# Kernel optimization log

Measured on AMD Instinct MI355X. Metric: run time of the kernel, lower is better.

The kernel has to match this reference:

```python
import jax, jax.numpy as jnp
import numpy as np

B, TQ, TKV = 2, 2048, 2048
Q_IN, KV_IN, D_MODEL, N_HEADS = 1024, 1024, 1024, 16
D_HEAD = D_MODEL // N_HEADS


def setup_inputs() -> dict:
    key = jax.random.key(0)
    ks = jax.random.split(key, 12)
    s_q = 1.0 / np.sqrt(Q_IN)
    s_kv = 1.0 / np.sqrt(KV_IN)
    s_o = 1.0 / np.sqrt(D_MODEL)
    return {
        "q": jax.random.normal(ks[0], (B, TQ, Q_IN), jnp.float32),
        "kv": jax.random.normal(ks[1], (B, TKV, KV_IN), jnp.float32),
        "mask": jnp.triu(jnp.ones((TQ, TKV), jnp.bool_), k=1),  # True = masked
        "Wq": jax.random.uniform(ks[2], (D_MODEL, Q_IN), jnp.float32, -s_q, s_q),
        "bq": jax.random.uniform(ks[3], (D_MODEL,), jnp.float32, -s_q, s_q),
        "Wk": jax.random.uniform(ks[4], (D_HEAD, KV_IN), jnp.float32, -s_kv, s_kv),
        "bk": jax.random.uniform(ks[5], (D_HEAD,), jnp.float32, -s_kv, s_kv),
        "Wv": jax.random.uniform(ks[6], (D_HEAD, KV_IN), jnp.float32, -s_kv, s_kv),
        "bv": jax.random.uniform(ks[7], (D_HEAD,), jnp.float32, -s_kv, s_kv),
        "Wo": jax.random.uniform(ks[8], (D_MODEL, D_MODEL), jnp.float32, -s_o, s_o),
        "bo": jax.random.uniform(ks[9], (D_MODEL,), jnp.float32, -s_o, s_o),
    }


def reference(q, kv, mask, Wq, bq, Wk, bk, Wv, bv, Wo, bo):
    b, tq, _ = q.shape
    scale = jnp.sqrt(jnp.asarray(D_HEAD, q.dtype))
    # Q: [B, H, Tq, Dh]; K/V: single shared head [B, Tkv, Dh]
    Q = (q @ Wq.T + bq).reshape(b, tq, N_HEADS, D_HEAD).transpose(0, 2, 1, 3)
    K = kv @ Wk.T + bk
    V = kv @ Wv.T + bv
    scores = jnp.einsum("bhqd,bkd->bhqk", Q, K) / scale
    scores = jnp.where(mask[None, None, :, :], -jnp.inf, scores)
    attn_weights = jax.nn.softmax(scores, axis=-1)  # dropout is identity (eval / p=0)
    attended = jnp.einsum("bhqk,bkd->bhqd", attn_weights, V)
    attended = attended.transpose(0, 2, 1, 3).reshape(b, tq, D_MODEL)
    out = attended @ Wo.T + bo
    return out, attn_weights
```

## Files before the change

### kernel.cpp

```cpp
#include <hip/hip_runtime.h>

#define BATCH 2
#define TQ 2048
#define TKV 2048
#define DMODEL 1024
#define NHEADS 16
#define DHEAD 64
#define KIN 1024

typedef __attribute__((ext_vector_type(4))) float f32x4;
typedef __attribute__((ext_vector_type(8))) short bf16x8;

#define MFMA16(a, b, c) __builtin_amdgcn_mfma_f32_16x16x32_bf16(a, b, c, 0, 0, 0)

__device__ inline short f2bf(float f) {
    unsigned u = __builtin_bit_cast(unsigned, f);
    unsigned r = u + 0x7FFFu + ((u >> 16) & 1u);
    return (short)(r >> 16);
}
__device__ inline bf16x8 cvt8v(f32x4 lo, f32x4 hi) {
    bf16x8 r;
    r[0] = f2bf(lo[0]); r[1] = f2bf(lo[1]); r[2] = f2bf(lo[2]); r[3] = f2bf(lo[3]);
    r[4] = f2bf(hi[0]); r[5] = f2bf(hi[1]); r[6] = f2bf(hi[2]); r[7] = f2bf(hi[3]);
    return r;
}

template<bool A_F32, bool OUT_F32>
__global__ __launch_bounds__(256) void gemm_bt_bias(
    const void* __restrict__ Av, const float* __restrict__ B,
    const float* __restrict__ bias, void* __restrict__ Cv,
    int M, int N, int K)
{
    __shared__ short As[128 * 40];
    __shared__ short Bs[128 * 40];
    const int tid = threadIdx.x;
    const int lane = tid & 63, wave = tid >> 6;
    const int quad = lane >> 4, l16 = lane & 15;
    const int wm = wave & 1, wn = wave >> 1;
    const int mBase = blockIdx.x * 128, nBase = blockIdx.y * 128;

    f32x4 acc[4][4];
#pragma unroll
    for (int i = 0; i < 4; i++)
#pragma unroll
        for (int j = 0; j < 4; j++) acc[i][j] = (f32x4){0.f, 0.f, 0.f, 0.f};

    const int r0 = tid >> 2;
    const int c0 = (tid & 3) * 8;

    for (int k0 = 0; k0 < K; k0 += 32) {
        bf16x8 a0, a1, b0, b1;
        if constexpr (A_F32) {
            const float* Af = (const float*)Av;
            const f32x4* p0 = (const f32x4*)&Af[(size_t)(mBase + r0) * K + k0 + c0];
            const f32x4* p1 = (const f32x4*)&Af[(size_t)(mBase + r0 + 64) * K + k0 + c0];
            a0 = cvt8v(p0[0], p0[1]);
            a1 = cvt8v(p1[0], p1[1]);
        } else {
            const short* Ab = (const short*)Av;
            a0 = *(const bf16x8*)&Ab[(size_t)(mBase + r0) * K + k0 + c0];
            a1 = *(const bf16x8*)&Ab[(size_t)(mBase + r0 + 64) * K + k0 + c0];
        }
        {
            const f32x4* q0 = (const f32x4*)&B[(size_t)(nBase + r0) * K + k0 + c0];
            const f32x4* q1 = (const f32x4*)&B[(size_t)(nBase + r0 + 64) * K + k0 + c0];
            b0 = cvt8v(q0[0], q0[1]);
            b1 = cvt8v(q1[0], q1[1]);
        }
        __syncthreads();
        *(bf16x8*)&As[r0 * 40 + c0] = a0;
        *(bf16x8*)&As[(r0 + 64) * 40 + c0] = a1;
        *(bf16x8*)&Bs[r0 * 40 + c0] = b0;
        *(bf16x8*)&Bs[(r0 + 64) * 40 + c0] = b1;
        __syncthreads();
        bf16x8 af[4], bfr[4];
#pragma unroll
        for (int mt = 0; mt < 4; mt++)
            af[mt] = *(const bf16x8*)&As[(wm * 64 + mt * 16 + l16) * 40 + quad * 8];
#pragma unroll
        for (int nt = 0; nt < 4; nt++)
            bfr[nt] = *(const bf16x8*)&Bs[(wn * 64 + nt * 16 + l16) * 40 + quad * 8];
#pragma unroll
        for (int mt = 0; mt < 4; mt++)
#pragma unroll
            for (int nt = 0; nt < 4; nt++)
                acc[mt][nt] = MFMA16(af[mt], bfr[nt], acc[mt][nt]);
    }

#pragma unroll
    for (int nt = 0; nt < 4; nt++) {
        int col = nBase + wn * 64 + nt * 16 + l16;
        float bv = bias[col];
#pragma unroll
        for (int mt = 0; mt < 4; mt++) {
            int row = mBase + wm * 64 + mt * 16 + quad * 4;
#pragma unroll
            for (int r = 0; r < 4; r++) {
                float val = acc[mt][nt][r] + bv;
                size_t idx = (size_t)(row + r) * N + col;
                if constexpr (OUT_F32) ((float*)Cv)[idx] = val;
                else                   ((short*)Cv)[idx] = f2bf(val);
            }
        }
    }
}

__global__ __launch_bounds__(256) void kvproj(
    const float* __restrict__ A,
    const float* __restrict__ Wk, const float* __restrict__ bkp,
    const float* __restrict__ Wv, const float* __restrict__ bvp,
    short* __restrict__ Kout,
    short* __restrict__ Vt)
{
    const int K = KIN;
    __shared__ short As[128 * 40];
    __shared__ short Bs[128 * 40];
    const int tid = threadIdx.x;
    const int lane = tid & 63, wave = tid >> 6;
    const int quad = lane >> 4, l16 = lane & 15;
    const int wm = wave & 1, wn = wave >> 1;
    const int mBase = blockIdx.x * 128;

    f32x4 acc[4][4];
#pragma unroll
    for (int i = 0; i < 4; i++)
#pragma unroll
        for (int j = 0; j < 4; j++) acc[i][j] = (f32x4){0.f, 0.f, 0.f, 0.f};

    const int r0 = tid >> 2;
    const int c0 = (tid & 3) * 8;

    for (int k0 = 0; k0 < K; k0 += 32) {
        const f32x4* p0 = (const f32x4*)&A[(size_t)(mBase + r0) * K + k0 + c0];
        const f32x4* p1 = (const f32x4*)&A[(size_t)(mBase + r0 + 64) * K + k0 + c0];
        const f32x4* q0 = (const f32x4*)&Wk[(size_t)r0 * K + k0 + c0];
        const f32x4* q1 = (const f32x4*)&Wv[(size_t)r0 * K + k0 + c0];
        bf16x8 a0 = cvt8v(p0[0], p0[1]);
        bf16x8 a1 = cvt8v(p1[0], p1[1]);
        bf16x8 b0 = cvt8v(q0[0], q0[1]);
        bf16x8 b1 = cvt8v(q1[0], q1[1]);
        __syncthreads();
        *(bf16x8*)&As[r0 * 40 + c0] = a0;
        *(bf16x8*)&As[(r0 + 64) * 40 + c0] = a1;
        *(bf16x8*)&Bs[r0 * 40 + c0] = b0;
        *(bf16x8*)&Bs[(r0 + 64) * 40 + c0] = b1;
        __syncthreads();
        bf16x8 af[4], bfr[4];
#pragma unroll
        for (int mt = 0; mt < 4; mt++)
            af[mt] = *(const bf16x8*)&As[(wm * 64 + mt * 16 + l16) * 40 + quad * 8];
#pragma unroll
        for (int nt = 0; nt < 4; nt++)
            bfr[nt] = *(const bf16x8*)&Bs[(wn * 64 + nt * 16 + l16) * 40 + quad * 8];
#pragma unroll
        for (int mt = 0; mt < 4; mt++)
#pragma unroll
            for (int nt = 0; nt < 4; nt++)
                acc[mt][nt] = MFMA16(af[mt], bfr[nt], acc[mt][nt]);
    }

#pragma unroll
    for (int nt = 0; nt < 4; nt++) {
        int n = wn * 64 + nt * 16 + l16;
        float bv = (n < 64) ? bkp[n] : bvp[n - 64];
#pragma unroll
        for (int mt = 0; mt < 4; mt++) {
            int row = mBase + wm * 64 + mt * 16 + quad * 4;
#pragma unroll
            for (int r = 0; r < 4; r++) {
                short v = f2bf(acc[mt][nt][r] + bv);
                int m = row + r;
                if (n < 64) {
                    Kout[(size_t)m * 64 + n] = v;
                } else {
                    int b = m >> 11, t = m & 2047;
                    Vt[((size_t)(b * 64 + (n - 64))) * 2048 + t] = v;
                }
            }
        }
    }
}

__global__ __launch_bounds__(256) void attn_core(
    const short* __restrict__ Qbuf,
    const short* __restrict__ Kbuf,
    const short* __restrict__ Vt,
    float* __restrict__ attnW,
    short* __restrict__ attOut)
{
    const int blk = blockIdx.x;
    const int qb = blk & 31;
    const int h = (blk >> 5) & 15;
    const int b = blk >> 9;
    const int lane = threadIdx.x & 63, wave = threadIdx.x >> 6;
    const int quad = lane >> 4, l16 = lane & 15;
    const int qrow0 = qb * 64 + wave * 16;

    __shared__ short EsAll[4][16 * 72];
    __shared__ float PsAll[4][16 * 68];
    short* Es = &EsAll[wave][0];
    float* Ps = &PsAll[wave][0];

    const short* qp = Qbuf + (size_t)(b * TQ + qrow0 + l16) * DMODEL + h * 64;
    bf16x8 aq[2];
    aq[0] = *(const bf16x8*)(qp + quad * 8);
    aq[1] = *(const bf16x8*)(qp + 32 + quad * 8);

    const short* Kb = Kbuf + (size_t)b * TKV * DHEAD;
    const short* Vb = Vt + (size_t)b * DHEAD * TKV;

    f32x4 attacc[4];
#pragma unroll
    for (int i = 0; i < 4; i++) attacc[i] = (f32x4){0.f, 0.f, 0.f, 0.f};
    float rowsum[4] = {0.f, 0.f, 0.f, 0.f};

    for (int kb = 0; kb <= qb; ++kb) {
        f32x4 s[4];
#pragma unroll
        for (int i = 0; i < 4; i++) s[i] = (f32x4){0.f, 0.f, 0.f, 0.f};
#pragma unroll
        for (int nt = 0; nt < 4; nt++) {
            const short* kp = Kb + (size_t)(kb * 64 + nt * 16 + l16) * DHEAD + quad * 8;
            bf16x8 k0 = *(const bf16x8*)kp;
            bf16x8 k1 = *(const bf16x8*)(kp + 32);
            s[nt] = MFMA16(aq[0], k0, s[nt]);
            s[nt] = MFMA16(aq[1], k1, s[nt]);
        }
        const bool diag = (kb == qb);
#pragma unroll
        for (int nt = 0; nt < 4; nt++) {
            int col = kb * 64 + nt * 16 + l16;
#pragma unroll
            for (int r = 0; r < 4; r++) {
                int row = qrow0 + quad * 4 + r;
                float e = (diag && col > row) ? 0.f : __expf(s[nt][r] * 0.125f);
                rowsum[r] += e;
                Es[(quad * 4 + r) * 72 + nt * 16 + l16] = f2bf(e);
            }
        }
        __syncthreads();
        bf16x8 ae0 = *(const bf16x8*)&Es[l16 * 72 + quad * 8];
        bf16x8 ae1 = *(const bf16x8*)&Es[l16 * 72 + 32 + quad * 8];
#pragma unroll
        for (int dt = 0; dt < 4; dt++) {
            const short* vp = Vb + (size_t)(dt * 16 + l16) * TKV + kb * 64 + quad * 8;
            bf16x8 v0 = *(const bf16x8*)vp;
            bf16x8 v1 = *(const bf16x8*)(vp + 32);
            attacc[dt] = MFMA16(ae0, v0, attacc[dt]);
            attacc[dt] = MFMA16(ae1, v1, attacc[dt]);
        }
        __syncthreads();
    }

#pragma unroll
    for (int r = 0; r < 4; r++) {
#pragma unroll
        for (int m = 1; m < 16; m <<= 1) rowsum[r] += __shfl_xor(rowsum[r], m, 64);
    }
    float rinv[4];
#pragma unroll
    for (int r = 0; r < 4; r++) rinv[r] = 1.f / rowsum[r];

#pragma unroll
    for (int dt = 0; dt < 4; dt++) {
#pragma unroll
        for (int r = 0; r < 4; r++) {
            size_t idx = (size_t)(b * TQ + qrow0 + quad * 4 + r) * DMODEL + h * 64 + dt * 16 + l16;
            attOut[idx] = f2bf(attacc[dt][r] * rinv[r]);
        }
    }

    float* Wrow = attnW + (size_t)(b * NHEADS + h) * TQ * TKV;
    const int srow = lane >> 2;
    const int sc = (lane & 3) * 16;
    const f32x4 zz = {0.f, 0.f, 0.f, 0.f};

    for (int kb = 0; kb < TKV / 64; ++kb) {
        float* gp = Wrow + (size_t)(qrow0 + srow) * TKV + kb * 64 + sc;
        if (kb > qb) {
            ((f32x4*)gp)[0] = zz; ((f32x4*)gp)[1] = zz;
            ((f32x4*)gp)[2] = zz; ((f32x4*)gp)[3] = zz;
        } else {
            f32x4 s[4];
#pragma unroll
            for (int i = 0; i < 4; i++) s[i] = (f32x4){0.f, 0.f, 0.f, 0.f};
#pragma unroll
            for (int nt = 0; nt < 4; nt++) {
                const short* kp = Kb + (size_t)(kb * 64 + nt * 16 + l16) * DHEAD + quad * 8;
                bf16x8 k0 = *(const bf16x8*)kp;
                bf16x8 k1 = *(const bf16x8*)(kp + 32);
                s[nt] = MFMA16(aq[0], k0, s[nt]);
                s[nt] = MFMA16(aq[1], k1, s[nt]);
            }
            const bool diag = (kb == qb);
#pragma unroll
            for (int nt = 0; nt < 4; nt++) {
                int col = kb * 64 + nt * 16 + l16;
#pragma unroll
                for (int r = 0; r < 4; r++) {
                    int row = qrow0 + quad * 4 + r;
                    float e = (diag && col > row) ? 0.f
                              : __expf(s[nt][r] * 0.125f) * rinv[r];
                    Ps[(quad * 4 + r) * 68 + nt * 16 + l16] = e;
                }
            }
            __syncthreads();
            f32x4 w0 = ((const f32x4*)&Ps[srow * 68 + sc])[0];
            f32x4 w1 = ((const f32x4*)&Ps[srow * 68 + sc])[1];
            f32x4 w2 = ((const f32x4*)&Ps[srow * 68 + sc])[2];
            f32x4 w3 = ((const f32x4*)&Ps[srow * 68 + sc])[3];
            ((f32x4*)gp)[0] = w0; ((f32x4*)gp)[1] = w1;
            ((f32x4*)gp)[2] = w2; ((f32x4*)gp)[3] = w3;
            __syncthreads();
        }
    }
}

extern "C" void kernel_launch(void* const* d_in, const int* in_sizes, int n_in,
                              void* d_out, int out_size, void* d_ws, size_t ws_size,
                              hipStream_t stream) {
    const float* q  = (const float*)d_in[0];
    const float* kv = (const float*)d_in[1];
    const float* Wq = (const float*)d_in[3];
    const float* bq = (const float*)d_in[4];
    const float* Wk = (const float*)d_in[5];
    const float* bk = (const float*)d_in[6];
    const float* Wv = (const float*)d_in[7];
    const float* bv = (const float*)d_in[8];
    const float* Wo = (const float*)d_in[9];
    const float* bo = (const float*)d_in[10];

    float* out   = (float*)d_out;
    float* attnW = out + (size_t)BATCH * TQ * DMODEL;

    short* Qbuf = (short*)d_ws;
    short* Kbuf = Qbuf + (size_t)BATCH * TQ * DMODEL;
    short* Vtb  = Kbuf + (size_t)BATCH * TKV * DHEAD;
    short* Att  = Vtb + (size_t)BATCH * DHEAD * TKV;

    dim3 blk(256);
    gemm_bt_bias<true, false><<<dim3(32, 8), blk, 0, stream>>>(
        q, Wq, bq, Qbuf, BATCH * TQ, DMODEL, KIN);
    kvproj<<<dim3(32, 1), blk, 0, stream>>>(kv, Wk, bk, Wv, bv, Kbuf, Vtb);
    attn_core<<<dim3(BATCH * NHEADS * (TQ / 64)), blk, 0, stream>>>(
        Qbuf, Kbuf, Vtb, attnW, Att);
    gemm_bt_bias<false, true><<<dim3(32, 8), blk, 0, stream>>>(
        Att, Wo, bo, out, BATCH * TQ, DMODEL, DMODEL);
}
```

Baseline: 1.056 ms.

## Shrink GEMM tiles, reverse attention block order, drop barriers, nontemporal weight stores

The projection GEMMs shrink to 128x64 tiles and kvproj to 64-row tiles, doubling grid sizes so more blocks fill the CUs. Attention blocks are launched heaviest-first by reversing the query-block index. The per-wave shared buffers are aliased and the block-wide barriers between per-wave stages are removed. Attention-weight writes become nontemporal row-strided stores. Removing barriers relies on each wave touching only its own shared region, and the smaller tiles re-read operands more often.

```diff
diff --git a/kernel.cpp b/kernel.cpp
--- a/kernel.cpp
+++ b/kernel.cpp
@@ -26,30 +26,32 @@
 }
 
 template<bool A_F32, bool OUT_F32>
-__global__ __launch_bounds__(256) void gemm_bt_bias(
+__global__ __launch_bounds__(256, 2) void gemm_bt_bias(
     const void* __restrict__ Av, const float* __restrict__ B,
     const float* __restrict__ bias, void* __restrict__ Cv,
     int M, int N, int K)
 {
     __shared__ short As[128 * 40];
-    __shared__ short Bs[128 * 40];
+    __shared__ short Bs[64 * 40];
     const int tid = threadIdx.x;
     const int lane = tid & 63, wave = tid >> 6;
     const int quad = lane >> 4, l16 = lane & 15;
     const int wm = wave & 1, wn = wave >> 1;
-    const int mBase = blockIdx.x * 128, nBase = blockIdx.y * 128;
-
-    f32x4 acc[4][4];
+    const int mBase = blockIdx.x * 128, nBase = blockIdx.y * 64;
+
+    f32x4 acc[4][2];
 #pragma unroll
     for (int i = 0; i < 4; i++)
 #pragma unroll
-        for (int j = 0; j < 4; j++) acc[i][j] = (f32x4){0.f, 0.f, 0.f, 0.f};
+        for (int j = 0; j < 2; j++) acc[i][j] = (f32x4){0.f, 0.f, 0.f, 0.f};
 
     const int r0 = tid >> 2;
     const int c0 = (tid & 3) * 8;
+    const int rB = tid & 63;
+    const int cB = (tid >> 6) * 8;
 
     for (int k0 = 0; k0 < K; k0 += 32) {
-        bf16x8 a0, a1, b0, b1;
+        bf16x8 a0, a1, b0;
         if constexpr (A_F32) {
             const float* Af = (const float*)Av;
             const f32x4* p0 = (const f32x4*)&Af[(size_t)(mBase + r0) * K + k0 + c0];
@@ -62,34 +64,31 @@
             a1 = *(const bf16x8*)&Ab[(size_t)(mBase + r0 + 64) * K + k0 + c0];
         }
         {
-            const f32x4* q0 = (const f32x4*)&B[(size_t)(nBase + r0) * K + k0 + c0];
-            const f32x4* q1 = (const f32x4*)&B[(size_t)(nBase + r0 + 64) * K + k0 + c0];
+            const f32x4* q0 = (const f32x4*)&B[(size_t)(nBase + rB) * K + k0 + cB];
             b0 = cvt8v(q0[0], q0[1]);
-            b1 = cvt8v(q1[0], q1[1]);
         }
         __syncthreads();
         *(bf16x8*)&As[r0 * 40 + c0] = a0;
         *(bf16x8*)&As[(r0 + 64) * 40 + c0] = a1;
-        *(bf16x8*)&Bs[r0 * 40 + c0] = b0;
-        *(bf16x8*)&Bs[(r0 + 64) * 40 + c0] = b1;
+        *(bf16x8*)&Bs[rB * 40 + cB] = b0;
         __syncthreads();
-        bf16x8 af[4], bfr[4];
+        bf16x8 af[4], bfr[2];
 #pragma unroll
         for (int mt = 0; mt < 4; mt++)
             af[mt] = *(const bf16x8*)&As[(wm * 64 + mt * 16 + l16) * 40 + quad * 8];
 #pragma unroll
-        for (int nt = 0; nt < 4; nt++)
-            bfr[nt] = *(const bf16x8*)&Bs[(wn * 64 + nt * 16 + l16) * 40 + quad * 8];
+        for (int nt = 0; nt < 2; nt++)
+            bfr[nt] = *(const bf16x8*)&Bs[(wn * 32 + nt * 16 + l16) * 40 + quad * 8];
 #pragma unroll
         for (int mt = 0; mt < 4; mt++)
 #pragma unroll
-            for (int nt = 0; nt < 4; nt++)
+            for (int nt = 0; nt < 2; nt++)
                 acc[mt][nt] = MFMA16(af[mt], bfr[nt], acc[mt][nt]);
     }
 
 #pragma unroll
-    for (int nt = 0; nt < 4; nt++) {
-        int col = nBase + wn * 64 + nt * 16 + l16;
+    for (int nt = 0; nt < 2; nt++) {
+        int col = nBase + wn * 32 + nt * 16 + l16;
         float bv = bias[col];
 #pragma unroll
         for (int mt = 0; mt < 4; mt++) {
@@ -113,47 +112,46 @@
     short* __restrict__ Vt)
 {
     const int K = KIN;
-    __shared__ short As[128 * 40];
+    __shared__ short As[64 * 40];
     __shared__ short Bs[128 * 40];
     const int tid = threadIdx.x;
     const int lane = tid & 63, wave = tid >> 6;
     const int quad = lane >> 4, l16 = lane & 15;
     const int wm = wave & 1, wn = wave >> 1;
-    const int mBase = blockIdx.x * 128;
-
-    f32x4 acc[4][4];
-#pragma unroll
-    for (int i = 0; i < 4; i++)
+    const int mBase = blockIdx.x * 64;
+
+    f32x4 acc[2][4];
+#pragma unroll
+    for (int i = 0; i < 2; i++)
 #pragma unroll
         for (int j = 0; j < 4; j++) acc[i][j] = (f32x4){0.f, 0.f, 0.f, 0.f};
 
+    const int rA = tid & 63;
+    const int cA = (tid >> 6) * 8;
     const int r0 = tid >> 2;
     const int c0 = (tid & 3) * 8;
 
     for (int k0 = 0; k0 < K; k0 += 32) {
-        const f32x4* p0 = (const f32x4*)&A[(size_t)(mBase + r0) * K + k0 + c0];
-        const f32x4* p1 = (const f32x4*)&A[(size_t)(mBase + r0 + 64) * K + k0 + c0];
+        const f32x4* p0 = (const f32x4*)&A[(size_t)(mBase + rA) * K + k0 + cA];
         const f32x4* q0 = (const f32x4*)&Wk[(size_t)r0 * K + k0 + c0];
         const f32x4* q1 = (const f32x4*)&Wv[(size_t)r0 * K + k0 + c0];
         bf16x8 a0 = cvt8v(p0[0], p0[1]);
-        bf16x8 a1 = cvt8v(p1[0], p1[1]);
         bf16x8 b0 = cvt8v(q0[0], q0[1]);
         bf16x8 b1 = cvt8v(q1[0], q1[1]);
         __syncthreads();
-        *(bf16x8*)&As[r0 * 40 + c0] = a0;
-        *(bf16x8*)&As[(r0 + 64) * 40 + c0] = a1;
+        *(bf16x8*)&As[rA * 40 + cA] = a0;
         *(bf16x8*)&Bs[r0 * 40 + c0] = b0;
         *(bf16x8*)&Bs[(r0 + 64) * 40 + c0] = b1;
         __syncthreads();
-        bf16x8 af[4], bfr[4];
-#pragma unroll
-        for (int mt = 0; mt < 4; mt++)
-            af[mt] = *(const bf16x8*)&As[(wm * 64 + mt * 16 + l16) * 40 + quad * 8];
+        bf16x8 af[2], bfr[4];
+#pragma unroll
+        for (int mt = 0; mt < 2; mt++)
+            af[mt] = *(const bf16x8*)&As[(wm * 32 + mt * 16 + l16) * 40 + quad * 8];
 #pragma unroll
         for (int nt = 0; nt < 4; nt++)
             bfr[nt] = *(const bf16x8*)&Bs[(wn * 64 + nt * 16 + l16) * 40 + quad * 8];
 #pragma unroll
-        for (int mt = 0; mt < 4; mt++)
+        for (int mt = 0; mt < 2; mt++)
 #pragma unroll
             for (int nt = 0; nt < 4; nt++)
                 acc[mt][nt] = MFMA16(af[mt], bfr[nt], acc[mt][nt]);
@@ -164,8 +162,8 @@
         int n = wn * 64 + nt * 16 + l16;
         float bv = (n < 64) ? bkp[n] : bvp[n - 64];
 #pragma unroll
-        for (int mt = 0; mt < 4; mt++) {
-            int row = mBase + wm * 64 + mt * 16 + quad * 4;
+        for (int mt = 0; mt < 2; mt++) {
+            int row = mBase + wm * 32 + mt * 16 + quad * 4;
 #pragma unroll
             for (int r = 0; r < 4; r++) {
                 short v = f2bf(acc[mt][nt][r] + bv);
@@ -173,8 +171,8 @@
                 if (n < 64) {
                     Kout[(size_t)m * 64 + n] = v;
                 } else {
-                    int b = m >> 11, t = m & 2047;
-                    Vt[((size_t)(b * 64 + (n - 64))) * 2048 + t] = v;
+                    int bb = m >> 11, t = m & 2047;
+                    Vt[((size_t)(bb * 64 + (n - 64))) * 2048 + t] = v;
                 }
             }
         }
@@ -189,17 +187,16 @@
     short* __restrict__ attOut)
 {
     const int blk = blockIdx.x;
-    const int qb = blk & 31;
+    const int qb = 31 - (blk & 31);
     const int h = (blk >> 5) & 15;
     const int b = blk >> 9;
     const int lane = threadIdx.x & 63, wave = threadIdx.x >> 6;
     const int quad = lane >> 4, l16 = lane & 15;
     const int qrow0 = qb * 64 + wave * 16;
 
-    __shared__ short EsAll[4][16 * 72];
     __shared__ float PsAll[4][16 * 68];
-    short* Es = &EsAll[wave][0];
     float* Ps = &PsAll[wave][0];
+    short* Es = (short*)Ps;
 
     const short* qp = Qbuf + (size_t)(b * TQ + qrow0 + l16) * DMODEL + h * 64;
     bf16x8 aq[2];
@@ -238,7 +235,6 @@
                 Es[(quad * 4 + r) * 72 + nt * 16 + l16] = f2bf(e);
             }
         }
-        __syncthreads();
         bf16x8 ae0 = *(const bf16x8*)&Es[l16 * 72 + quad * 8];
         bf16x8 ae1 = *(const bf16x8*)&Es[l16 * 72 + 32 + quad * 8];
 #pragma unroll
@@ -249,7 +245,6 @@
             attacc[dt] = MFMA16(ae0, v0, attacc[dt]);
             attacc[dt] = MFMA16(ae1, v1, attacc[dt]);
         }
-        __syncthreads();
     }
 
 #pragma unroll
@@ -271,15 +266,17 @@
     }
 
     float* Wrow = attnW + (size_t)(b * NHEADS + h) * TQ * TKV;
-    const int srow = lane >> 2;
-    const int sc = (lane & 3) * 16;
+    const int srow = lane >> 4;
+    const int sc = (lane & 15) * 4;
     const f32x4 zz = {0.f, 0.f, 0.f, 0.f};
 
     for (int kb = 0; kb < TKV / 64; ++kb) {
-        float* gp = Wrow + (size_t)(qrow0 + srow) * TKV + kb * 64 + sc;
         if (kb > qb) {
-            ((f32x4*)gp)[0] = zz; ((f32x4*)gp)[1] = zz;
-            ((f32x4*)gp)[2] = zz; ((f32x4*)gp)[3] = zz;
+#pragma unroll
+            for (int i = 0; i < 4; i++) {
+                float* gp = Wrow + (size_t)(qrow0 + i * 4 + srow) * TKV + kb * 64 + sc;
+                __builtin_nontemporal_store(zz, (f32x4*)gp);
+            }
         } else {
             f32x4 s[4];
 #pragma unroll
@@ -304,14 +301,12 @@
                     Ps[(quad * 4 + r) * 68 + nt * 16 + l16] = e;
                 }
             }
-            __syncthreads();
-            f32x4 w0 = ((const f32x4*)&Ps[srow * 68 + sc])[0];
-            f32x4 w1 = ((const f32x4*)&Ps[srow * 68 + sc])[1];
-            f32x4 w2 = ((const f32x4*)&Ps[srow * 68 + sc])[2];
-            f32x4 w3 = ((const f32x4*)&Ps[srow * 68 + sc])[3];
-            ((f32x4*)gp)[0] = w0; ((f32x4*)gp)[1] = w1;
-            ((f32x4*)gp)[2] = w2; ((f32x4*)gp)[3] = w3;
-            __syncthreads();
+#pragma unroll
+            for (int i = 0; i < 4; i++) {
+                f32x4 w = *(const f32x4*)&Ps[(i * 4 + srow) * 68 + sc];
+                float* gp = Wrow + (size_t)(qrow0 + i * 4 + srow) * TKV + kb * 64 + sc;
+                __builtin_nontemporal_store(w, (f32x4*)gp);
+            }
         }
     }
 }
@@ -339,11 +334,11 @@
     short* Att  = Vtb + (size_t)BATCH * DHEAD * TKV;
 
     dim3 blk(256);
-    gemm_bt_bias<true, false><<<dim3(32, 8), blk, 0, stream>>>(
+    gemm_bt_bias<true, false><<<dim3(32, 16), blk, 0, stream>>>(
         q, Wq, bq, Qbuf, BATCH * TQ, DMODEL, KIN);
-    kvproj<<<dim3(32, 1), blk, 0, stream>>>(kv, Wk, bk, Wv, bv, Kbuf, Vtb);
+    kvproj<<<dim3(64, 1), blk, 0, stream>>>(kv, Wk, bk, Wv, bv, Kbuf, Vtb);
     attn_core<<<dim3(BATCH * NHEADS * (TQ / 64)), blk, 0, stream>>>(
         Qbuf, Kbuf, Vtb, attnW, Att);
-    gemm_bt_bias<false, true><<<dim3(32, 8), blk, 0, stream>>>(
+    gemm_bt_bias<false, true><<<dim3(32, 16), blk, 0, stream>>>(
         Att, Wo, bo, out, BATCH * TQ, DMODEL, DMODEL);
 }
```

Measured after the change: 966.5 us. 1.09x faster.
